# Performance work log

Measured on AMD Instinct MI355X. Metric: run time of the kernel, lower is better.

Reference implementation:

```python
import jax, jax.numpy as jnp
import numpy as np

N = 524288   # predicate-expression nodes
M = N // 2   # binary-formula nodes
L = 50       # self.length
VOCAB = 100  # max_embeddings
OUT = 3 * L + 5  # output_size = 155


def _attention(x, W_att, b_att):
    # x: [B, k, L]. torch Attention: softmax over the stacked-args axis, weighted sum.
    logits = jnp.einsum('bkl,lo->bko', x, W_att) + b_att   # [B, k, 1]
    a = jax.nn.softmax(logits, axis=1)
    return jnp.sum(a * x, axis=1)                           # [B, L]


def setup_inputs() -> dict:
    key = jax.random.key(0)
    ks = jax.random.split(key, 20)
    s = 0.05
    inp = {
        'pe': jax.random.normal(ks[0], (VOCAB, L), jnp.float32),
        've': jax.random.normal(ks[1], (VOCAB, L), jnp.float32),
        'oe': jax.random.normal(ks[2], (VOCAB, L), jnp.float32),
        'W_pred': jax.random.normal(ks[3], (6 * L, L), jnp.float32) * s,
        'b_pred': jax.random.normal(ks[4], (L,), jnp.float32) * s,
        'W_bin': jax.random.normal(ks[5], (3 * L, L), jnp.float32) * s,
        'b_bin': jax.random.normal(ks[6], (L,), jnp.float32) * s,
        'W_un': jax.random.normal(ks[7], (L, L), jnp.float32) * s,
        'b_un': jax.random.normal(ks[8], (L,), jnp.float32) * s,
        'W_univ': jax.random.normal(ks[9], (L, L), jnp.float32) * s,
        'b_univ': jax.random.normal(ks[10], (L,), jnp.float32) * s,
        'W_att': jax.random.normal(ks[11], (L, 1), jnp.float32) * s,
        'b_att': jax.random.normal(ks[12], (1,), jnp.float32) * s,
        'W_fin': jax.random.normal(ks[13], (L, OUT), jnp.float32) * s,
        'b_fin': jax.random.normal(ks[14], (OUT,), jnp.float32) * s,
        'pred_ids': jax.random.randint(ks[15], (N,), 0, VOCAB),
        'var_ids': jax.random.randint(ks[16], (N, 5), 0, VOCAB),
        'op_ids': jax.random.randint(ks[17], (M,), 0, VOCAB),
    }
    return inp


def reference(pe, ve, oe, W_pred, b_pred, W_bin, b_bin, W_un, b_un,
              W_univ, b_univ, W_att, b_att, W_fin, b_fin,
              pred_ids, var_ids, op_ids):
    # visit_predicate_expression, batched: [predicate_emb, 5 arg embs] -> [N, 6, L]
    args = jnp.concatenate([pe[pred_ids][:, None, :], ve[var_ids]], axis=1)
    h_pred = (jax.nn.relu(args.reshape(N, 6 * L) @ W_pred + b_pred)
              + _attention(args, W_att, b_att))                      # [N, L]

    # visit_binary_formula, batched over adjacent pairs: [left, op, right]
    ops = jnp.stack([h_pred[0::2], oe[op_ids], h_pred[1::2]], axis=1)  # [M, 3, L]
    h_bin = (jax.nn.relu(ops.reshape(M, 3 * L) @ W_bin + b_bin)
             + _attention(ops, W_att, b_att))                         # [M, L]

    # visit_unary_formula, then universal quantified formula
    h_un = jax.nn.relu(h_bin @ W_un + b_un)
    h_q = jax.nn.relu(h_un @ W_univ + b_univ)

    # final projection: forward() -> self.final(...)
    return h_q @ W_fin + b_fin  # [M, OUT]
```

## Files before the change

### kernel.cpp

```cpp
#include <hip/hip_runtime.h>
#include <hip/hip_fp16.h>

#define LDIM 50
#define MBIN 262144
#define ODIM 155
#define VOCABSZ 100

typedef _Float16 f16x4 __attribute__((ext_vector_type(4)));
typedef _Float16 f16x2 __attribute__((ext_vector_type(2)));
typedef float    f32x4 __attribute__((ext_vector_type(4)));

static __device__ __forceinline__ __half2 relu2(__half2 a) {
    f16x2 av; __builtin_memcpy(&av, &a, sizeof(av));
    const f16x2 zv = {(_Float16)0.0f, (_Float16)0.0f};
    f16x2 r = __builtin_elementwise_max(av, zv);
    __half2 out; __builtin_memcpy(&out, &r, sizeof(out));
    return out;
}

#define H_TBL  0
#define H_TO   44800
#define H_WC   54800
#define H_WU   62224
#define H_WV   66576
#define H_WF   70928
#define F_LG   40960

#define LB_WC   118784
#define LB_WU   133632
#define LB_WV   142336
#define LB_WF   118784
#define LB_SW   140544
#define LB_OP   151040
#define LB_W0   153088
#define LB_W2   155136
#define LB_W1   157184
#define LB_BU   159232
#define LB_BV   159432
#define LB_BF   159632
#define LB_LG   160256
#define LB_WATT 161456
#define LDS_BYTES 161568

__global__ __launch_bounds__(256) void precompute_kernel(
    const float* __restrict__ pe, const float* __restrict__ ve, const float* __restrict__ oe,
    const float* __restrict__ W_pred, const float* __restrict__ b_pred,
    const float* __restrict__ W_bin, const float* __restrict__ b_bin,
    const float* __restrict__ W_un, const float* __restrict__ W_univ,
    const float* __restrict__ W_fin,
    const float* __restrict__ W_att, const float* __restrict__ b_att,
    float* __restrict__ ws)
{
    __half* wsh = (__half*)ws;
    const int bid = blockIdx.x, tid = threadIdx.x;
    if (bid < 150) {
        const int row = bid*4 + (tid >> 6);
        const int t = tid & 63;
        const int s = row / VOCABSZ, v = row % VOCABSZ;
        if (t < 56) {
            float acc = 0.0f;
            if (t < 50) {
                acc = (s == 0) ? b_pred[t] : 0.0f;
                const float* E = (s == 0) ? pe : ve;
#pragma unroll
                for (int e = 0; e < 50; ++e)
                    acc += E[v*50 + e] * W_pred[(s*50 + e)*50 + t];
            }
            wsh[H_TBL + row*56 + t] = __float2half_rn(acc);
        }
    } else if (bid < 152) {
        const int which = bid - 150;
        const float* E = which ? ve : pe;
        const int base = H_TBL + (600 + which*100) * 56;
        for (int idx = tid; idx < 5600; idx += 256) {
            const int r = idx / 56, c = idx % 56;
            wsh[base + idx] = __float2half_rn((c < 50) ? E[r*50 + c] : 0.0f);
        }
    } else if (bid < 177) {
        const int v = (bid - 152)*4 + (tid >> 6);
        const int t = tid & 63;
        if (t < 50) {
            float acc = b_bin[t];
#pragma unroll
            for (int e = 0; e < 50; ++e)
                acc += oe[v*50 + e] * W_bin[(50 + e)*50 + t];
            wsh[H_TO + (v*50 + t)*2]     = __float2half_rn(acc);
            wsh[H_TO + (v*50 + t)*2 + 1] = __float2half_rn(oe[v*50 + t]);
        }
    } else if (bid == 177) {
        const int n = tid & 63, kc = tid >> 6;
        for (int k = kc*29; k < kc*29 + 29; ++k) {
            float val = 0.0f;
            if (n < 50) {
                if (k < 50)       val = W_bin[k*50 + n];
                else if (k < 100) val = W_bin[(100 + k - 50)*50 + n];
            }
            wsh[H_WC + n*116 + k] = __float2half_rn(val);
        }
    } else if (bid == 178) {
        const int n = tid & 63;
        const int half = tid >> 7;
        const int kc = (tid >> 6) & 1;
        const float* W = half ? W_univ : W_un;
        const int base = half ? H_WV : H_WU;
        for (int k = kc*34; k < kc*34 + 34; ++k) {
            float val = (n < 50 && k < 50) ? W[k*50 + n] : 0.0f;
            wsh[base + n*68 + k] = __float2half_rn(val);
        }
    } else if (bid == 179) {
        for (int idx = tid; idx < 10880; idx += 256) {
            const int n = idx % 160, k = idx / 160;
            float val = (n < ODIM && k < 50) ? W_fin[k*ODIM + n] : 0.0f;
            wsh[H_WF + n*68 + k] = __float2half_rn(val);
        }
    } else {
        for (int g = tid; g < 300; g += 256) {
            const int which = g / VOCABSZ, v = g % VOCABSZ;
            const float* E = (which == 0) ? pe : ((which == 1) ? ve : oe);
            float acc = b_att[0];
#pragma unroll
            for (int e = 0; e < 50; ++e)
                acc += E[v*50 + e] * W_att[e];
            ws[F_LG + g] = acc;
        }
    }
}

__device__ __forceinline__ float build_node(
    int p, const int* __restrict__ v, __half2 e02, const __half2* __restrict__ ek2,
    __half2 invs, const char* __restrict__ ldsraw, __half2* __restrict__ h2out)
{
    const uint4* Tq = (const uint4*)ldsraw;
    const __half2* wattl = (const __half2*)(ldsraw + LB_WATT);
    const __half2 z2 = __floats2half2_rn(0.0f, 0.0f);
    __half2 lacc = z2;
#pragma unroll
    for (int g = 0; g < 7; ++g) {
        uint4 ul = Tq[p*7 + g];
        uint4 up = Tq[(600 + p)*7 + g];
        __half2 lin[4], num[4];
#pragma unroll
        for (int k = 0; k < 4; ++k) {
            lin[k] = ((const __half2*)&ul)[k];
            num[k] = __hmul2(e02, ((const __half2*)&up)[k]);
        }
#pragma unroll
        for (int s = 0; s < 5; ++s) {
            uint4 ua = Tq[((s+1)*VOCABSZ + v[s])*7 + g];
            uint4 uv = Tq[(700 + v[s])*7 + g];
#pragma unroll
            for (int k = 0; k < 4; ++k) {
                lin[k] = __hadd2(lin[k], ((const __half2*)&ua)[k]);
                num[k] = __hfma2(ek2[s], ((const __half2*)&uv)[k], num[k]);
            }
        }
#pragma unroll
        for (int k = 0; k < 4; ++k) {
            const __half2 h = __hfma2(num[k], invs, relu2(lin[k]));
            h2out[g*4 + k] = h;
            lacc = __hfma2(h, wattl[g*4 + k], lacc);
        }
    }
    return __low2float(lacc) + __high2float(lacc);
}

__global__ __launch_bounds__(512)
void fused_kernel(
    const float* __restrict__ W_att, const float* __restrict__ b_att,
    const float* __restrict__ b_un, const float* __restrict__ b_univ,
    const float* __restrict__ b_fin,
    const int* __restrict__ pred_ids, const int* __restrict__ var_ids,
    const int* __restrict__ op_ids,
    const float* __restrict__ ws, float* __restrict__ out)
{
    __shared__ __align__(16) char ldsraw[LDS_BYTES];
    const __half* wsh = (const __half*)ws;
    const int tid = threadIdx.x;
    const int w = tid >> 6, l = tid & 63;
    const int lr = l & 15, q = l >> 4;
    const int jbase = blockIdx.x * 512;

    int*   opl = (int*)(ldsraw + LB_OP);
    float* w0l = (float*)(ldsraw + LB_W0);
    float* w2l = (float*)(ldsraw + LB_W2);
    float* w1l = (float*)(ldsraw + LB_W1);
    float* bul = (float*)(ldsraw + LB_BU);
    float* bvl = (float*)(ldsraw + LB_BV);
    float* bfl = (float*)(ldsraw + LB_BF);
    float* lgl = (float*)(ldsraw + LB_LG);

    {
        const uint4* s = (const uint4*)wsh;
        uint4* d = (uint4*)ldsraw;
        for (int i = tid; i < 5600; i += 512) d[i] = s[i];
        const uint2* sc = (const uint2*)(wsh + H_WC);
        uint2* dc = (uint2*)(ldsraw + LB_WC);
        for (int i = tid; i < 1856; i += 512) dc[i] = sc[i];
        const uint2* su = (const uint2*)(wsh + H_WU);
        uint2* du = (uint2*)(ldsraw + LB_WU);
        for (int i = tid; i < 1088; i += 512) du[i] = su[i];
        const uint2* sv = (const uint2*)(wsh + H_WV);
        uint2* dv = (uint2*)(ldsraw + LB_WV);
        for (int i = tid; i < 1088; i += 512) dv[i] = sv[i];
        if (tid < 300) lgl[tid] = ws[F_LG + tid];
        if (tid < LDIM) { bul[tid] = b_un[tid]; bvl[tid] = b_univ[tid]; }
        if (tid < ODIM) bfl[tid] = b_fin[tid];
        if (tid >= 256 && tid < 284) {
            const int i = tid - 256;
            const float x = (2*i < 50)   ? W_att[2*i]   : 0.0f;
            const float y = (2*i+1 < 50) ? W_att[2*i+1] : 0.0f;
            ((__half2*)(ldsraw + LB_WATT))[i] = __floats2half2_rn(x, y);
        }
    }
    __syncthreads();

    const int j = jbase + tid;
    int vA[5], vB[5];
    const int pA = pred_ids[2*j], pB = pred_ids[2*j+1];
#pragma unroll
    for (int s = 0; s < 5; ++s) { vA[s] = var_ids[(2*j)*5 + s]; vB[s] = var_ids[(2*j+1)*5 + s]; }
    const int op = op_ids[j];

    float ekA[5], ekB[5];
    const float e0A = __expf(lgl[pA]);
    const float e0B = __expf(lgl[pB]);
    float denA = e0A, denB = e0B;
#pragma unroll
    for (int s = 0; s < 5; ++s) {
        ekA[s] = __expf(lgl[VOCABSZ + vA[s]]); denA += ekA[s];
        ekB[s] = __expf(lgl[VOCABSZ + vB[s]]); denB += ekB[s];
    }
    const float invA = 1.0f / denA, invB = 1.0f / denB;
    const float batt = b_att[0];

    __half2 ek2A[5], ek2B[5];
#pragma unroll
    for (int s = 0; s < 5; ++s) {
        ek2A[s] = __float2half2_rn(ekA[s]);
        ek2B[s] = __float2half2_rn(ekB[s]);
    }

    __half2 hA2[28], hB2[28];
    const float w0 = __expf(batt + build_node(pA, vA, __float2half2_rn(e0A), ek2A,
                                              __float2half2_rn(invA), ldsraw, hA2));
    const float w2 = __expf(batt + build_node(pB, vB, __float2half2_rn(e0B), ek2B,
                                              __float2half2_rn(invB), ldsraw, hB2));
    const float w1 = __expf(lgl[2*VOCABSZ + op]);
    const float inv2 = 1.0f / (w0 + w1 + w2);

    __syncthreads();

    {
        __half2* Hrow = (__half2*)ldsraw + tid*58;
#pragma unroll
        for (int i = 0; i < 25; ++i) Hrow[i] = hA2[i];
#pragma unroll
        for (int i = 0; i < 25; ++i) Hrow[25+i] = hB2[i];
        const __half2 z = __floats2half2_rn(0.0f, 0.0f);
#pragma unroll
        for (int i = 50; i < 58; ++i) Hrow[i] = z;
        opl[tid] = op;
        w0l[tid] = w0*inv2; w2l[tid] = w2*inv2; w1l[tid] = w1*inv2;
    }

    const _Float16* Hp  = (const _Float16*)ldsraw;
    __half*         Hw  = (__half*)ldsraw;
    f32x4 C[4][4];

    {
        const _Float16* Wcp = (const _Float16*)(ldsraw + LB_WC);
#pragma unroll
        for (int mt = 0; mt < 4; ++mt)
#pragma unroll
            for (int nt = 0; nt < 4; ++nt)
                C[mt][nt] = (f32x4){0.f, 0.f, 0.f, 0.f};
#pragma unroll
        for (int kk = 0; kk < 7; ++kk) {
            f16x4 bf[4];
#pragma unroll
            for (int nt = 0; nt < 4; ++nt)
                bf[nt] = *(const f16x4*)(Wcp + (nt*16 + lr)*116 + kk*16 + q*4);
#pragma unroll
            for (int mt = 0; mt < 4; ++mt) {
                f16x4 a = *(const f16x4*)(Hp + (w*64 + mt*16 + lr)*116 + kk*16 + q*4);
#pragma unroll
                for (int nt = 0; nt < 4; ++nt)
                    C[mt][nt] = __builtin_amdgcn_mfma_f32_16x16x16f16(a, bf[nt], C[mt][nt], 0, 0, 0);
            }
        }
        const __half2* TOg = (const __half2*)(wsh + H_TO);
#pragma unroll
        for (int mt = 0; mt < 4; ++mt)
#pragma unroll
            for (int nt = 0; nt < 4; ++nt) {
                const int d = nt*16 + lr;
#pragma unroll
                for (int r = 0; r < 4; ++r) {
                    const int node = w*64 + mt*16 + q*4 + r;
                    float v = 0.0f;
                    if (d < LDIM) {
                        const int opn = opl[node];
                        const float2 to = __half22float2(TOg[opn*LDIM + d]);
                        const float hA = __half2float(Hp[node*116 + d]);
                        const float hB = __half2float(Hp[node*116 + 50 + d]);
                        v = fmaxf(C[mt][nt][r] + to.x, 0.0f)
                          + w0l[node]*hA + w2l[node]*hB + w1l[node]*to.y;
                    }
                    C[mt][nt][r] = v;
                }
            }
    }
    __syncthreads();
#pragma unroll
    for (int mt = 0; mt < 4; ++mt)
#pragma unroll
        for (int nt = 0; nt < 4; ++nt) {
            const int d = nt*16 + lr;
#pragma unroll
            for (int r = 0; r < 4; ++r)
                Hw[(w*64 + mt*16 + q*4 + r)*68 + d] = __float2half(C[mt][nt][r]);
        }

    {
        const _Float16* Wup = (const _Float16*)(ldsraw + LB_WU);
#pragma unroll
        for (int mt = 0; mt < 4; ++mt)
#pragma unroll
            for (int nt = 0; nt < 4; ++nt)
                C[mt][nt] = (f32x4){0.f, 0.f, 0.f, 0.f};
#pragma unroll
        for (int kk = 0; kk < 4; ++kk) {
            f16x4 bf[4];
#pragma unroll
            for (int nt = 0; nt < 4; ++nt)
                bf[nt] = *(const f16x4*)(Wup + (nt*16 + lr)*68 + kk*16 + q*4);
#pragma unroll
            for (int mt = 0; mt < 4; ++mt) {
                f16x4 a = *(const f16x4*)(Hp + (w*64 + mt*16 + lr)*68 + kk*16 + q*4);
#pragma unroll
                for (int nt = 0; nt < 4; ++nt)
                    C[mt][nt] = __builtin_amdgcn_mfma_f32_16x16x16f16(a, bf[nt], C[mt][nt], 0, 0, 0);
            }
        }
    }
    __syncthreads();
    {
#pragma unroll
        for (int mt = 0; mt < 4; ++mt)
#pragma unroll
            for (int nt = 0; nt < 4; ++nt) {
                const int d = nt*16 + lr;
#pragma unroll
                for (int r = 0; r < 4; ++r) {
                    const float v = (d < LDIM) ? fmaxf(C[mt][nt][r] + bul[d], 0.0f) : 0.0f;
                    Hw[(w*64 + mt*16 + q*4 + r)*68 + d] = __float2half(v);
                }
            }
        const uint2* sf = (const uint2*)(wsh + H_WF);
        uint2* df = (uint2*)(ldsraw + LB_WF);
        for (int i = tid; i < 2720; i += 512) df[i] = sf[i];
    }

    {
        const _Float16* Wvp = (const _Float16*)(ldsraw + LB_WV);
#pragma unroll
        for (int mt = 0; mt < 4; ++mt)
#pragma unroll
            for (int nt = 0; nt < 4; ++nt)
                C[mt][nt] = (f32x4){0.f, 0.f, 0.f, 0.f};
#pragma unroll
        for (int kk = 0; kk < 4; ++kk) {
            f16x4 bf[4];
#pragma unroll
            for (int nt = 0; nt < 4; ++nt)
                bf[nt] = *(const f16x4*)(Wvp + (nt*16 + lr)*68 + kk*16 + q*4);
#pragma unroll
            for (int mt = 0; mt < 4; ++mt) {
                f16x4 a = *(const f16x4*)(Hp + (w*64 + mt*16 + lr)*68 + kk*16 + q*4);
#pragma unroll
                for (int nt = 0; nt < 4; ++nt)
                    C[mt][nt] = __builtin_amdgcn_mfma_f32_16x16x16f16(a, bf[nt], C[mt][nt], 0, 0, 0);
            }
        }
#pragma unroll
        for (int mt = 0; mt < 4; ++mt)
#pragma unroll
            for (int nt = 0; nt < 4; ++nt) {
                const int d = nt*16 + lr;
#pragma unroll
                for (int r = 0; r < 4; ++r) {
                    const float v = (d < LDIM) ? fmaxf(C[mt][nt][r] + bvl[d], 0.0f) : 0.0f;
                    Hw[(w*64 + mt*16 + q*4 + r)*68 + d] = __float2half(v);
                }
            }
    }
    __syncthreads();

    {
        const _Float16* Wfp = (const _Float16*)(ldsraw + LB_WF);
        float* sww = (float*)(ldsraw + LB_SW) + w*272;
        for (int nt = 0; nt < 10; ++nt) {
            f16x4 bf[4];
#pragma unroll
            for (int kk = 0; kk < 4; ++kk)
                bf[kk] = *(const f16x4*)(Wfp + (nt*16 + lr)*68 + kk*16 + q*4);
            const int o = nt*16 + lr;
#pragma unroll
            for (int mt = 0; mt < 4; ++mt) {
                f32x4 c = (f32x4){0.f, 0.f, 0.f, 0.f};
#pragma unroll
                for (int kk = 0; kk < 4; ++kk) {
                    f16x4 a = *(const f16x4*)(Hp + (w*64 + mt*16 + lr)*68 + kk*16 + q*4);
                    c = __builtin_amdgcn_mfma_f32_16x16x16f16(a, bf[kk], c, 0, 0, 0);
                }
#pragma unroll
                for (int r = 0; r < 4; ++r)
                    sww[(q*4 + r)*17 + lr] = c[r] + ((o < ODIM) ? bfl[o] : 0.0f);
                float* gb = out + (size_t)(jbase + w*64 + mt*16) * ODIM + nt*16;
#pragma unroll
                for (int it = 0; it < 4; ++it) {
                    const int row = it*4 + q;
                    if (nt*16 + lr < ODIM)
                        gb[row*ODIM + lr] = sww[row*17 + lr];
                }
            }
        }
    }
}

extern "C" void kernel_launch(void* const* d_in, const int* in_sizes, int n_in,
                              void* d_out, int out_size, void* d_ws, size_t ws_size,
                              hipStream_t stream) {
    const float* pe     = (const float*)d_in[0];
    const float* ve     = (const float*)d_in[1];
    const float* oe     = (const float*)d_in[2];
    const float* W_pred = (const float*)d_in[3];
    const float* b_pred = (const float*)d_in[4];
    const float* W_bin  = (const float*)d_in[5];
    const float* b_bin  = (const float*)d_in[6];
    const float* W_un   = (const float*)d_in[7];
    const float* b_un   = (const float*)d_in[8];
    const float* W_univ = (const float*)d_in[9];
    const float* b_univ = (const float*)d_in[10];
    const float* W_att  = (const float*)d_in[11];
    const float* b_att  = (const float*)d_in[12];
    const float* W_fin  = (const float*)d_in[13];
    const float* b_fin  = (const float*)d_in[14];
    const int* pred_ids = (const int*)d_in[15];
    const int* var_ids  = (const int*)d_in[16];
    const int* op_ids   = (const int*)d_in[17];
    float* out = (float*)d_out;
    float* ws  = (float*)d_ws;

    precompute_kernel<<<181, 256, 0, stream>>>(pe, ve, oe, W_pred, b_pred,
                                               W_bin, b_bin, W_un, W_univ, W_fin,
                                               W_att, b_att, ws);
    fused_kernel<<<MBIN/512, 512, 0, stream>>>(W_att, b_att, b_un, b_univ, b_fin,
                                               pred_ids, var_ids, op_ids, ws, out);
}
```

Measured before the change: 322.9 us.

## Stream per-wave 16-row slabs through MLP chain and read tables from global

The gather table and W_fin are no longer staged in LDS; lanes read them directly from global memory. Each wave now runs the bin, unary, universal and final matmul chain on 16-row chunks in its own small LDS slab, which removes the block-wide barriers between stages. Total LDS per block drops from about 161KB to about 72KB, so more blocks may fit per CU. The cost is that the random embedding-table gathers and the W_fin loads now go through the cache hierarchy instead of LDS, and the 16-row chunks give less MFMA reuse per B-fragment load.

```diff
diff --git a/kernel.cpp b/kernel.cpp
--- a/kernel.cpp
+++ b/kernel.cpp
@@ -26,21 +26,20 @@
 #define H_WF   70928
 #define F_LG   40960
 
-#define LB_WC   118784
-#define LB_WU   133632
-#define LB_WV   142336
-#define LB_WF   118784
-#define LB_SW   140544
-#define LB_OP   151040
-#define LB_W0   153088
-#define LB_W2   155136
-#define LB_W1   157184
-#define LB_BU   159232
-#define LB_BV   159432
-#define LB_BF   159632
-#define LB_LG   160256
-#define LB_WATT 161456
-#define LDS_BYTES 161568
+#define LB_SLAB 0
+#define LB_WC   29696
+#define LB_WU   44544
+#define LB_WV   53248
+#define LB_OP   61952
+#define LB_W0   64000
+#define LB_W2   66048
+#define LB_W1   68096
+#define LB_BU   70144
+#define LB_BV   70400
+#define LB_BF   70656
+#define LB_LG   71296
+#define LB_WATT 72512
+#define LDS_BYTES 72640
 
 __global__ __launch_bounds__(256) void precompute_kernel(
     const float* __restrict__ pe, const float* __restrict__ ve, const float* __restrict__ oe,
@@ -128,16 +127,15 @@
 
 __device__ __forceinline__ float build_node(
     int p, const int* __restrict__ v, __half2 e02, const __half2* __restrict__ ek2,
-    __half2 invs, const char* __restrict__ ldsraw, __half2* __restrict__ h2out)
+    __half2 invs, const uint4* __restrict__ tq, const __half2* __restrict__ wattl,
+    __half2* __restrict__ h2out)
 {
-    const uint4* Tq = (const uint4*)ldsraw;
-    const __half2* wattl = (const __half2*)(ldsraw + LB_WATT);
     const __half2 z2 = __floats2half2_rn(0.0f, 0.0f);
     __half2 lacc = z2;
 #pragma unroll
     for (int g = 0; g < 7; ++g) {
-        uint4 ul = Tq[p*7 + g];
-        uint4 up = Tq[(600 + p)*7 + g];
+        uint4 ul = tq[p*7 + g];
+        uint4 up = tq[(600 + p)*7 + g];
         __half2 lin[4], num[4];
 #pragma unroll
         for (int k = 0; k < 4; ++k) {
@@ -146,8 +144,8 @@
         }
 #pragma unroll
         for (int s = 0; s < 5; ++s) {
-            uint4 ua = Tq[((s+1)*VOCABSZ + v[s])*7 + g];
-            uint4 uv = Tq[(700 + v[s])*7 + g];
+            uint4 ua = tq[((s+1)*VOCABSZ + v[s])*7 + g];
+            uint4 uv = tq[(700 + v[s])*7 + g];
 #pragma unroll
             for (int k = 0; k < 4; ++k) {
                 lin[k] = __hadd2(lin[k], ((const __half2*)&ua)[k]);
@@ -190,18 +188,15 @@
     float* lgl = (float*)(ldsraw + LB_LG);
 
     {
-        const uint4* s = (const uint4*)wsh;
-        uint4* d = (uint4*)ldsraw;
-        for (int i = tid; i < 5600; i += 512) d[i] = s[i];
-        const uint2* sc = (const uint2*)(wsh + H_WC);
-        uint2* dc = (uint2*)(ldsraw + LB_WC);
-        for (int i = tid; i < 1856; i += 512) dc[i] = sc[i];
-        const uint2* su = (const uint2*)(wsh + H_WU);
-        uint2* du = (uint2*)(ldsraw + LB_WU);
-        for (int i = tid; i < 1088; i += 512) du[i] = su[i];
-        const uint2* sv = (const uint2*)(wsh + H_WV);
-        uint2* dv = (uint2*)(ldsraw + LB_WV);
-        for (int i = tid; i < 1088; i += 512) dv[i] = sv[i];
+        const uint4* sc = (const uint4*)(wsh + H_WC);
+        uint4* dc = (uint4*)(ldsraw + LB_WC);
+        for (int i = tid; i < 928; i += 512) dc[i] = sc[i];
+        const uint4* su = (const uint4*)(wsh + H_WU);
+        uint4* du = (uint4*)(ldsraw + LB_WU);
+        for (int i = tid; i < 544; i += 512) du[i] = su[i];
+        const uint4* sv = (const uint4*)(wsh + H_WV);
+        uint4* dv = (uint4*)(ldsraw + LB_WV);
+        for (int i = tid; i < 544; i += 512) dv[i] = sv[i];
         if (tid < 300) lgl[tid] = ws[F_LG + tid];
         if (tid < LDIM) { bul[tid] = b_un[tid]; bvl[tid] = b_univ[tid]; }
         if (tid < ODIM) bfl[tid] = b_fin[tid];
@@ -240,188 +235,153 @@
         ek2B[s] = __float2half2_rn(ekB[s]);
     }
 
+    const uint4* tq = (const uint4*)wsh;
+    const __half2* wattl = (const __half2*)(ldsraw + LB_WATT);
+
     __half2 hA2[28], hB2[28];
     const float w0 = __expf(batt + build_node(pA, vA, __float2half2_rn(e0A), ek2A,
-                                              __float2half2_rn(invA), ldsraw, hA2));
+                                              __float2half2_rn(invA), tq, wattl, hA2));
     const float w2 = __expf(batt + build_node(pB, vB, __float2half2_rn(e0B), ek2B,
-                                              __float2half2_rn(invB), ldsraw, hB2));
+                                              __float2half2_rn(invB), tq, wattl, hB2));
     const float w1 = __expf(lgl[2*VOCABSZ + op]);
     const float inv2 = 1.0f / (w0 + w1 + w2);
 
-    __syncthreads();
-
-    {
-        __half2* Hrow = (__half2*)ldsraw + tid*58;
-#pragma unroll
-        for (int i = 0; i < 25; ++i) Hrow[i] = hA2[i];
-#pragma unroll
-        for (int i = 0; i < 25; ++i) Hrow[25+i] = hB2[i];
-        const __half2 z = __floats2half2_rn(0.0f, 0.0f);
-#pragma unroll
-        for (int i = 50; i < 58; ++i) Hrow[i] = z;
-        opl[tid] = op;
-        w0l[tid] = w0*inv2; w2l[tid] = w2*inv2; w1l[tid] = w1*inv2;
-    }
-
-    const _Float16* Hp  = (const _Float16*)ldsraw;
-    __half*         Hw  = (__half*)ldsraw;
-    f32x4 C[4][4];
-
-    {
-        const _Float16* Wcp = (const _Float16*)(ldsraw + LB_WC);
-#pragma unroll
-        for (int mt = 0; mt < 4; ++mt)
-#pragma unroll
-            for (int nt = 0; nt < 4; ++nt)
-                C[mt][nt] = (f32x4){0.f, 0.f, 0.f, 0.f};
+    opl[tid] = op;
+    w0l[tid] = w0*inv2; w2l[tid] = w2*inv2; w1l[tid] = w1*inv2;
+
+    char* slab = ldsraw + LB_SLAB + w*3712;
+    const __half2* TOg = (const __half2*)(wsh + H_TO);
+    const _Float16* Wcp = (const _Float16*)(ldsraw + LB_WC);
+    const _Float16* Wup = (const _Float16*)(ldsraw + LB_WU);
+    const _Float16* Wvp = (const _Float16*)(ldsraw + LB_WV);
+    const _Float16* Wfg = (const _Float16*)(wsh + H_WF);
+
+    for (int c = 0; c < 4; ++c) {
+        if ((l >> 4) == c) {
+            uint* dst = (uint*)(slab + (l & 15)*232);
+#pragma unroll
+            for (int i = 0; i < 25; ++i) { uint u; __builtin_memcpy(&u, &hA2[i], 4); dst[i] = u; }
+#pragma unroll
+            for (int i = 0; i < 25; ++i) { uint u; __builtin_memcpy(&u, &hB2[i], 4); dst[25+i] = u; }
+#pragma unroll
+            for (int i = 50; i < 58; ++i) dst[i] = 0u;
+        }
+
+        f32x4 C1[4];
+#pragma unroll
+        for (int nt = 0; nt < 4; ++nt) C1[nt] = (f32x4){0.f, 0.f, 0.f, 0.f};
 #pragma unroll
         for (int kk = 0; kk < 7; ++kk) {
-            f16x4 bf[4];
-#pragma unroll
-            for (int nt = 0; nt < 4; ++nt)
-                bf[nt] = *(const f16x4*)(Wcp + (nt*16 + lr)*116 + kk*16 + q*4);
-#pragma unroll
-            for (int mt = 0; mt < 4; ++mt) {
-                f16x4 a = *(const f16x4*)(Hp + (w*64 + mt*16 + lr)*116 + kk*16 + q*4);
-#pragma unroll
-                for (int nt = 0; nt < 4; ++nt)
-                    C[mt][nt] = __builtin_amdgcn_mfma_f32_16x16x16f16(a, bf[nt], C[mt][nt], 0, 0, 0);
-            }
-        }
-        const __half2* TOg = (const __half2*)(wsh + H_TO);
-#pragma unroll
-        for (int mt = 0; mt < 4; ++mt)
+            f16x4 a = *(const f16x4*)(slab + lr*232 + kk*32 + q*8);
+#pragma unroll
+            for (int nt = 0; nt < 4; ++nt) {
+                f16x4 b = *(const f16x4*)((const char*)Wcp + (nt*16 + lr)*232 + kk*32 + q*8);
+                C1[nt] = __builtin_amdgcn_mfma_f32_16x16x16f16(a, b, C1[nt], 0, 0, 0);
+            }
+        }
+        {
+            const __half* sh = (const __half*)slab;
+            const int cb = c*16;
 #pragma unroll
             for (int nt = 0; nt < 4; ++nt) {
                 const int d = nt*16 + lr;
 #pragma unroll
                 for (int r = 0; r < 4; ++r) {
-                    const int node = w*64 + mt*16 + q*4 + r;
                     float v = 0.0f;
                     if (d < LDIM) {
-                        const int opn = opl[node];
+                        const int nw = w*64 + cb + q*4 + r;
+                        const int opn = opl[nw];
                         const float2 to = __half22float2(TOg[opn*LDIM + d]);
-                        const float hA = __half2float(Hp[node*116 + d]);
-                        const float hB = __half2float(Hp[node*116 + 50 + d]);
-                        v = fmaxf(C[mt][nt][r] + to.x, 0.0f)
-                          + w0l[node]*hA + w2l[node]*hB + w1l[node]*to.y;
+                        const float hAv = __half2float(sh[(q*4 + r)*116 + d]);
+                        const float hBv = __half2float(sh[(q*4 + r)*116 + 50 + d]);
+                        v = fmaxf(C1[nt][r] + to.x, 0.0f)
+                          + w0l[nw]*hAv + w2l[nw]*hBv + w1l[nw]*to.y;
                     }
-                    C[mt][nt][r] = v;
-                }
-            }
-    }
-    __syncthreads();
-#pragma unroll
-    for (int mt = 0; mt < 4; ++mt)
-#pragma unroll
-        for (int nt = 0; nt < 4; ++nt) {
-            const int d = nt*16 + lr;
-#pragma unroll
-            for (int r = 0; r < 4; ++r)
-                Hw[(w*64 + mt*16 + q*4 + r)*68 + d] = __float2half(C[mt][nt][r]);
-        }
-
-    {
-        const _Float16* Wup = (const _Float16*)(ldsraw + LB_WU);
-#pragma unroll
-        for (int mt = 0; mt < 4; ++mt)
+                    C1[nt][r] = v;
+                }
+            }
+            __half* shw = (__half*)slab;
 #pragma unroll
             for (int nt = 0; nt < 4; ++nt)
-                C[mt][nt] = (f32x4){0.f, 0.f, 0.f, 0.f};
-#pragma unroll
-        for (int kk = 0; kk < 4; ++kk) {
-            f16x4 bf[4];
-#pragma unroll
-            for (int nt = 0; nt < 4; ++nt)
-                bf[nt] = *(const f16x4*)(Wup + (nt*16 + lr)*68 + kk*16 + q*4);
-#pragma unroll
-            for (int mt = 0; mt < 4; ++mt) {
-                f16x4 a = *(const f16x4*)(Hp + (w*64 + mt*16 + lr)*68 + kk*16 + q*4);
-#pragma unroll
-                for (int nt = 0; nt < 4; ++nt)
-                    C[mt][nt] = __builtin_amdgcn_mfma_f32_16x16x16f16(a, bf[nt], C[mt][nt], 0, 0, 0);
-            }
-        }
-    }
-    __syncthreads();
-    {
-#pragma unroll
-        for (int mt = 0; mt < 4; ++mt)
+#pragma unroll
+                for (int r = 0; r < 4; ++r)
+                    shw[(q*4 + r)*116 + nt*16 + lr] = __float2half(C1[nt][r]);
+        }
+
+        {
+            f32x4 C2[4];
+#pragma unroll
+            for (int nt = 0; nt < 4; ++nt) C2[nt] = (f32x4){0.f, 0.f, 0.f, 0.f};
+#pragma unroll
+            for (int kk = 0; kk < 4; ++kk) {
+                f16x4 a = *(const f16x4*)(slab + lr*232 + kk*32 + q*8);
+#pragma unroll
+                for (int nt = 0; nt < 4; ++nt) {
+                    f16x4 b = *(const f16x4*)((const char*)Wup + (nt*16 + lr)*136 + kk*32 + q*8);
+                    C2[nt] = __builtin_amdgcn_mfma_f32_16x16x16f16(a, b, C2[nt], 0, 0, 0);
+                }
+            }
+            __half* shw = (__half*)slab;
 #pragma unroll
             for (int nt = 0; nt < 4; ++nt) {
                 const int d = nt*16 + lr;
 #pragma unroll
                 for (int r = 0; r < 4; ++r) {
-                    const float v = (d < LDIM) ? fmaxf(C[mt][nt][r] + bul[d], 0.0f) : 0.0f;
-                    Hw[(w*64 + mt*16 + q*4 + r)*68 + d] = __float2half(v);
-                }
-            }
-        const uint2* sf = (const uint2*)(wsh + H_WF);
-        uint2* df = (uint2*)(ldsraw + LB_WF);
-        for (int i = tid; i < 2720; i += 512) df[i] = sf[i];
-    }
-
-    {
-        const _Float16* Wvp = (const _Float16*)(ldsraw + LB_WV);
-#pragma unroll
-        for (int mt = 0; mt < 4; ++mt)
-#pragma unroll
-            for (int nt = 0; nt < 4; ++nt)
-                C[mt][nt] = (f32x4){0.f, 0.f, 0.f, 0.f};
-#pragma unroll
-        for (int kk = 0; kk < 4; ++kk) {
-            f16x4 bf[4];
-#pragma unroll
-            for (int nt = 0; nt < 4; ++nt)
-                bf[nt] = *(const f16x4*)(Wvp + (nt*16 + lr)*68 + kk*16 + q*4);
-#pragma unroll
-            for (int mt = 0; mt < 4; ++mt) {
-                f16x4 a = *(const f16x4*)(Hp + (w*64 + mt*16 + lr)*68 + kk*16 + q*4);
-#pragma unroll
-                for (int nt = 0; nt < 4; ++nt)
-                    C[mt][nt] = __builtin_amdgcn_mfma_f32_16x16x16f16(a, bf[nt], C[mt][nt], 0, 0, 0);
-            }
-        }
-#pragma unroll
-        for (int mt = 0; mt < 4; ++mt)
+                    const float v = (d < LDIM) ? fmaxf(C2[nt][r] + bul[d], 0.0f) : 0.0f;
+                    shw[(q*4 + r)*116 + d] = __float2half(v);
+                }
+            }
+        }
+
+        {
+            f32x4 C3[4];
+#pragma unroll
+            for (int nt = 0; nt < 4; ++nt) C3[nt] = (f32x4){0.f, 0.f, 0.f, 0.f};
+#pragma unroll
+            for (int kk = 0; kk < 4; ++kk) {
+                f16x4 a = *(const f16x4*)(slab + lr*232 + kk*32 + q*8);
+#pragma unroll
+                for (int nt = 0; nt < 4; ++nt) {
+                    f16x4 b = *(const f16x4*)((const char*)Wvp + (nt*16 + lr)*136 + kk*32 + q*8);
+                    C3[nt] = __builtin_amdgcn_mfma_f32_16x16x16f16(a, b, C3[nt], 0, 0, 0);
+                }
+            }
+            __half* shw = (__half*)slab;
 #pragma unroll
             for (int nt = 0; nt < 4; ++nt) {
                 const int d = nt*16 + lr;
 #pragma unroll
                 for (int r = 0; r < 4; ++r) {
-                    const float v = (d < LDIM) ? fmaxf(C[mt][nt][r] + bvl[d], 0.0f) : 0.0f;
-                    Hw[(w*64 + mt*16 + q*4 + r)*68 + d] = __float2half(v);
-                }
-            }
-    }
-    __syncthreads();
-
-    {
-        const _Float16* Wfp = (const _Float16*)(ldsraw + LB_WF);
-        float* sww = (float*)(ldsraw + LB_SW) + w*272;
-        for (int nt = 0; nt < 10; ++nt) {
-            f16x4 bf[4];
-#pragma unroll
-            for (int kk = 0; kk < 4; ++kk)
-                bf[kk] = *(const f16x4*)(Wfp + (nt*16 + lr)*68 + kk*16 + q*4);
-            const int o = nt*16 + lr;
-#pragma unroll
-            for (int mt = 0; mt < 4; ++mt) {
-                f32x4 c = (f32x4){0.f, 0.f, 0.f, 0.f};
+                    const float v = (d < LDIM) ? fmaxf(C3[nt][r] + bvl[d], 0.0f) : 0.0f;
+                    shw[(q*4 + r)*116 + d] = __float2half(v);
+                }
+            }
+        }
+
+        {
+            float* gb = out + (size_t)(jbase + w*64 + c*16) * ODIM;
+            for (int nt = 0; nt < 10; ++nt) {
+                f16x4 bf[4];
+#pragma unroll
+                for (int kk = 0; kk < 4; ++kk)
+                    bf[kk] = *(const f16x4*)((const char*)Wfg + (nt*16 + lr)*136 + kk*32 + q*8);
+                f32x4 c4 = (f32x4){0.f, 0.f, 0.f, 0.f};
 #pragma unroll
                 for (int kk = 0; kk < 4; ++kk) {
-                    f16x4 a = *(const f16x4*)(Hp + (w*64 + mt*16 + lr)*68 + kk*16 + q*4);
-                    c = __builtin_amdgcn_mfma_f32_16x16x16f16(a, bf[kk], c, 0, 0, 0);
-                }
+                    f16x4 a = *(const f16x4*)(slab + lr*232 + kk*32 + q*8);
+                    c4 = __builtin_amdgcn_mfma_f32_16x16x16f16(a, bf[kk], c4, 0, 0, 0);
+                }
+                const int o = nt*16 + lr;
+                const float bv = (o < ODIM) ? bfl[o] : 0.0f;
 #pragma unroll
                 for (int r = 0; r < 4; ++r)
-                    sww[(q*4 + r)*17 + lr] = c[r] + ((o < ODIM) ? bfl[o] : 0.0f);
-                float* gb = out + (size_t)(jbase + w*64 + mt*16) * ODIM + nt*16;
+                    *(float*)(slab + (q*4 + r)*232 + 128 + lr*4) = c4[r] + bv;
 #pragma unroll
                 for (int it = 0; it < 4; ++it) {
                     const int row = it*4 + q;
-                    if (nt*16 + lr < ODIM)
-                        gb[row*ODIM + lr] = sww[row*17 + lr];
+                    if (o < ODIM)
+                        gb[row*ODIM + nt*16 + lr] =
+                            *(const float*)(slab + row*232 + 128 + lr*4);
                 }
             }
         }
```

New measurement: 311.4 us. -3.6%, faster.
